# Kernel tuning notes

Measured on AMD Instinct MI355X. Metric: run time of the kernel, lower is better.

The kernel has to match this reference:

```python
import jax, jax.numpy as jnp
import numpy as np

NEG_SLOPE = 0.2


def gat_layer(x, src, dst, W, a_src, a_dst, bias, num_nodes, concat):
    """PyG-style GATConv (eval mode, self-loops already included in src/dst).
    x: [N, F_in]; W: [F_in, H*C]; a_src, a_dst: [H, C]; bias: [H*C] or [C].
    """
    H, C = a_src.shape
    h = (x @ W).reshape(num_nodes, H, C)                    # [N,H,C]
    alpha_s = jnp.einsum('nhc,hc->nh', h, a_src)            # [N,H]
    alpha_d = jnp.einsum('nhc,hc->nh', h, a_dst)            # [N,H]
    e = alpha_s[src] + alpha_d[dst]                         # [E,H]
    e = jnp.where(e > 0, e, NEG_SLOPE * e)                  # LeakyReLU(0.2)
    # segment softmax over destination nodes (numerically stable)
    m = jax.ops.segment_max(e, dst, num_segments=num_nodes)  # [N,H]
    m = jnp.where(jnp.isfinite(m), m, 0.0)
    ex = jnp.exp(e - m[dst])                                # [E,H]
    s = jax.ops.segment_sum(ex, dst, num_segments=num_nodes)  # [N,H]
    alpha = ex / (s[dst] + 1e-16)                           # [E,H]
    msg = h[src] * alpha[:, :, None]                        # [E,H,C]
    out = jax.ops.segment_sum(msg, dst, num_segments=num_nodes)  # [N,H,C]
    if concat:
        out = out.reshape(num_nodes, H * C)
    else:
        out = out.mean(axis=1)
    return out + bias


def _forward(x, edge_index, W1, a_src1, a_dst1, b1, W2, a_src2, a_dst2, b2):
    N = x.shape[0]
    loops = jnp.arange(N, dtype=edge_index.dtype)
    src = jnp.concatenate([edge_index[0], loops])
    dst = jnp.concatenate([edge_index[1], loops])
    h = gat_layer(x, src, dst, W1, a_src1, a_dst1, b1, N, concat=True)
    h = jax.nn.relu(h)  # dropout inactive in eval
    h = gat_layer(h, src, dst, W2, a_src2, a_dst2, b2, N, concat=False)
    return jax.nn.log_softmax(h, axis=1)


def setup_inputs() -> dict:
    key = jax.random.key(0)
    ks = jax.random.split(key, 10)
    N, E, F_in, Hid, H1, F_out = 100000, 1600000, 128, 64, 2, 7
    x = jax.random.normal(ks[0], (N, F_in), dtype=jnp.float32)
    edge_index = jax.random.randint(ks[1], (2, E), 0, N, dtype=jnp.int64)
    s1 = 1.0 / np.sqrt(F_in)
    W1 = jax.random.uniform(ks[2], (F_in, H1 * Hid), jnp.float32, -s1, s1)
    a_src1 = jax.random.uniform(ks[3], (H1, Hid), jnp.float32, -s1, s1)
    a_dst1 = jax.random.uniform(ks[4], (H1, Hid), jnp.float32, -s1, s1)
    b1 = jnp.zeros((H1 * Hid,), jnp.float32)
    s2 = 1.0 / np.sqrt(H1 * Hid)
    W2 = jax.random.uniform(ks[5], (H1 * Hid, F_out), jnp.float32, -s2, s2)
    a_src2 = jax.random.uniform(ks[6], (1, F_out), jnp.float32, -s2, s2)
    a_dst2 = jax.random.uniform(ks[7], (1, F_out), jnp.float32, -s2, s2)
    b2 = jnp.zeros((F_out,), jnp.float32)
    return {"x": x, "edge_index": edge_index, "W1": W1, "a_src1": a_src1,
            "a_dst1": a_dst1, "b1": b1, "W2": W2, "a_src2": a_src2,
            "a_dst2": a_dst2, "b2": b2}


def reference(x, edge_index, W1, a_src1, a_dst1, b1, W2, a_src2, a_dst2, b2):
    return _forward(x, edge_index, W1, a_src1, a_dst1, b1, W2, a_src2, a_dst2, b2)
```

## Files before the change

kernel.cpp:

```cpp
#include <hip/hip_runtime.h>
#include <hip/hip_bf16.h>

#define F_IN 128
#define HC   128
#define C1   64
#define F_OUT 7
#define H2S  8
#define BSH  9
#define BSZ  512
#define BINCH 8192
#define BCAP 12288

typedef __attribute__((ext_vector_type(8))) short short8;
typedef __attribute__((ext_vector_type(4))) float f32x4;
typedef __attribute__((ext_vector_type(2))) float f32x2;

__device__ __forceinline__ ushort f2bf(float f) {
    uint u = __builtin_bit_cast(uint, f);
    u = (u + 0x7FFFu + ((u >> 16) & 1u)) >> 16;
    return (ushort)u;
}

__device__ __forceinline__ int perm_col(int p_byte) {
    int slp = p_byte >> 3, j = p_byte & 7;
    int h = slp >> 3, sg = slp & 7;
    int lr = 2 * sg + (j >> 2), jj = j & 3;
    return 16 * (4 * h + jj) + lr;
}

__global__ __launch_bounds__(256) void k_cvt(
    const float* __restrict__ W1, ushort* __restrict__ Wsw,
    const float* __restrict__ W2, const float* __restrict__ b1,
    float* __restrict__ W2p, float* __restrict__ b1p)
{
    int b = blockIdx.x, t = threadIdx.x;
    if (b < 64) {
        int i = b * 256 + t;
        int k = i >> 7, n = i & 127;
        float v = W1[k * HC + n];
        int idx = n * 128 + (((k & ~7) ^ ((n & 7) << 3)) | (k & 7));
        Wsw[idx] = f2bf(v);
    } else {
        for (int i = t; i < 128 * F_OUT; i += 256) {
            int p = i / F_OUT, o = i - p * F_OUT;
            W2p[i] = W2[perm_col(p) * F_OUT + o];
        }
        if (t < 128) b1p[t] = b1[perm_col(t)];
    }
}

__global__ __launch_bounds__(256) void k_bingemm(
    const int* __restrict__ ei, int E, int Etot, int NBIN,
    int* __restrict__ bcnt, uint* __restrict__ binned,
    const float* __restrict__ x, const ushort* __restrict__ Wsw,
    const float* __restrict__ a_src, const float* __restrict__ a_dst,
    unsigned char* __restrict__ h1p, float* __restrict__ as1, float* __restrict__ ad1,
    int N)
{
    __shared__ __align__(16) char smem[128 * 128 * 2];
    const int t = threadIdx.x;

    if ((int)blockIdx.x < NBIN) {
        int* hist = (int*)smem;
        int* base = hist + 256;
        hist[t] = 0;
        __syncthreads();
        long c0 = (long)blockIdx.x * BINCH;
#pragma unroll
        for (int i = 0; i < BINCH / 256; ++i) {
            long e = c0 + t + i * 256;
            if (e < Etot) {
                int d = (e < E) ? ei[E + e] : (int)(e - E);
                atomicAdd(&hist[d >> BSH], 1);
            }
        }
        __syncthreads();
        base[t] = t * BCAP + ((hist[t] > 0) ? atomicAdd(&bcnt[t], hist[t]) : 0);
        __syncthreads();
#pragma unroll
        for (int i = 0; i < BINCH / 256; ++i) {
            long e = c0 + t + i * 256;
            if (e < Etot) {
                int s, d;
                if (e < E) { s = ei[e]; d = ei[E + e]; } else { s = (int)(e - E); d = s; }
                int bkt = d >> BSH;
                int pos = atomicAdd(&base[bkt], 1);
                if (pos < (bkt + 1) * BCAP)
                    binned[pos] = ((uint)s << BSH) | (uint)(d & (BSZ - 1));
            }
        }
    } else {
        ushort* Bs = (ushort*)smem;
        const int w = t >> 6, l = t & 63;
        const int lr = l & 15, hi = l >> 4;
        const int n0 = (blockIdx.x - NBIN) * 64;

        {
            const uint4* src = (const uint4*)Wsw;
            uint4* dst = (uint4*)Bs;
#pragma unroll
            for (int it = 0; it < 8; ++it) dst[t + it * 256] = src[t + it * 256];
        }
        __syncthreads();

        f32x4 acc[8];
#pragma unroll
        for (int j = 0; j < 8; ++j) acc[j] = (f32x4){0.f, 0.f, 0.f, 0.f};

        int arow = n0 + w * 16 + lr;
        if (arow >= N) arow = N - 1;
        const float* aptr = x + (size_t)arow * F_IN + hi * 8;

#pragma unroll
        for (int kt = 0; kt < 4; ++kt) {
            float4 f0 = *(const float4*)(aptr + kt * 32);
            float4 f1 = *(const float4*)(aptr + kt * 32 + 4);
            short8 a;
            a[0] = (short)f2bf(f0.x); a[1] = (short)f2bf(f0.y);
            a[2] = (short)f2bf(f0.z); a[3] = (short)f2bf(f0.w);
            a[4] = (short)f2bf(f1.x); a[5] = (short)f2bf(f1.y);
            a[6] = (short)f2bf(f1.z); a[7] = (short)f2bf(f1.w);
#pragma unroll
            for (int j = 0; j < 8; ++j) {
                int rn = 16 * j + lr;
                int kidx = (kt * 32 + hi * 8) ^ ((rn & 7) << 3);
                short8 b = *(const short8*)(Bs + rn * 128 + kidx);
                acc[j] = __builtin_amdgcn_mfma_f32_16x16x32_bf16(a, b, acc[j], 0, 0, 0);
            }
        }

        float as_[8], ad_[8];
#pragma unroll
        for (int j = 0; j < 8; ++j) {
            int hd = j >> 2;
            int c = 16 * (j & 3) + lr;
            as_[j] = a_src[hd * C1 + c];
            ad_[j] = a_dst[hd * C1 + c];
        }
#pragma unroll
        for (int i = 0; i < 4; ++i) {
            int r = n0 + w * 16 + hi * 4 + i;
            float ps0 = 0, ps1 = 0, pd0 = 0, pd1 = 0;
#pragma unroll
            for (int j = 0; j < 4; ++j) { ps0 += acc[j][i] * as_[j]; pd0 += acc[j][i] * ad_[j]; }
#pragma unroll
            for (int j = 4; j < 8; ++j) { ps1 += acc[j][i] * as_[j]; pd1 += acc[j][i] * ad_[j]; }
#pragma unroll
            for (int off = 1; off <= 8; off <<= 1) {
                ps0 += __shfl_xor(ps0, off, 64);
                ps1 += __shfl_xor(ps1, off, 64);
                pd0 += __shfl_xor(pd0, off, 64);
                pd1 += __shfl_xor(pd1, off, 64);
            }
            if (r < N) {
                int w0 = 0, w1 = 0;
                w0 = __builtin_amdgcn_cvt_pk_fp8_f32(acc[0][i], acc[1][i], w0, false);
                w0 = __builtin_amdgcn_cvt_pk_fp8_f32(acc[2][i], acc[3][i], w0, true);
                w1 = __builtin_amdgcn_cvt_pk_fp8_f32(acc[4][i], acc[5][i], w1, false);
                w1 = __builtin_amdgcn_cvt_pk_fp8_f32(acc[6][i], acc[7][i], w1, true);
                *(uint*)(h1p + (size_t)r * HC + lr * 4)      = (uint)w0;
                *(uint*)(h1p + (size_t)r * HC + 64 + lr * 4) = (uint)w1;
                if (lr == 0) {
                    as1[r * 2 + 0] = ps0; as1[r * 2 + 1] = ps1;
                    ad1[r * 2 + 0] = pd0; ad1[r * 2 + 1] = pd1;
                }
            }
        }
    }
}

__global__ __launch_bounds__(256) void k_fill(
    const uint* __restrict__ binned, const int* __restrict__ bcnt,
    int* __restrict__ rowptr, int* __restrict__ csr, int N, int NB)
{
    __shared__ int deg[BSZ];
    __shared__ int cur[BSZ];
    __shared__ int sc[256];
    int b = blockIdx.x, t = threadIdx.x;
    int cv = (t < NB) ? min(bcnt[t], BCAP) : 0;
    sc[t] = cv;
    __syncthreads();
    for (int off = 1; off < 256; off <<= 1) {
        int u = (t >= off) ? sc[t - off] : 0;
        __syncthreads();
        sc[t] += u;
        __syncthreads();
    }
    int total = sc[255];
    int s0 = (b > 0) ? sc[b - 1] : 0;
    int cntb = min(bcnt[b], BCAP);
    __syncthreads();

    int n0 = b << BSH;
    int nn = N - n0; if (nn > BSZ) nn = BSZ;
    deg[t] = 0; deg[t + 256] = 0;
    __syncthreads();
    const uint* bb = binned + (size_t)b * BCAP;
    for (int i = t; i < cntb; i += 256)
        atomicAdd(&deg[bb[i] & (BSZ - 1)], 1);
    __syncthreads();
    int d0 = deg[2 * t], d1 = deg[2 * t + 1];
    int ts = d0 + d1;
    sc[t] = ts;
    __syncthreads();
    for (int off = 1; off < 256; off <<= 1) {
        int u = (t >= off) ? sc[t - off] : 0;
        __syncthreads();
        sc[t] += u;
        __syncthreads();
    }
    int ex = sc[t] - ts + s0;
    if (2 * t < nn)     { rowptr[n0 + 2 * t]     = ex;      cur[2 * t]     = ex; }
    if (2 * t + 1 < nn) { rowptr[n0 + 2 * t + 1] = ex + d0; cur[2 * t + 1] = ex + d0; }
    __syncthreads();
    for (int i = t; i < cntb; i += 256) {
        uint en = bb[i];
        int pos = atomicAdd(&cur[en & (BSZ - 1)], 1);
        csr[pos] = (int)(en >> BSH);
    }
    if (b == 0 && t == 0) rowptr[N] = total;
}

__global__ __launch_bounds__(256) void k_aggr1_l2(
    const int* __restrict__ rowptr, const int* __restrict__ csr_src,
    const float* __restrict__ as1, const float* __restrict__ ad1,
    const unsigned char* __restrict__ h1p, const float* __restrict__ b1p,
    const float* __restrict__ W2p, const float* __restrict__ a_src2,
    const float* __restrict__ a_dst2,
    float* __restrict__ h2p, float* __restrict__ as2, float* __restrict__ ad2,
    int N)
{
    int w = threadIdx.x >> 6, l = threadIdx.x & 63;
    int q = l >> 4, sl = l & 15;
    int n = blockIdx.x * 16 + w * 4 + q;
    if (n >= N) return;
    const int h = sl >> 3;
    const int boff = sl * 8;
    float adv = ad1[n * 2 + h];
    int beg = rowptr[n], end = rowptr[n + 1];
    f32x2 ac01 = {0.f, 0.f}, ac23 = {0.f, 0.f}, ac45 = {0.f, 0.f}, ac67 = {0.f, 0.f};
    float s = 0.f;

    int i = beg;
    for (; i + 4 <= end; i += 4) {
        int sv[4]; float Av[4]; uint2 Hv[4];
#pragma unroll
        for (int j = 0; j < 4; ++j) sv[j] = csr_src[i + j];
#pragma unroll
        for (int j = 0; j < 4; ++j) Av[j] = as1[sv[j] * 2 + h];
#pragma unroll
        for (int j = 0; j < 4; ++j)
            Hv[j] = *(const uint2*)(h1p + (((size_t)(uint)sv[j]) << 7) + boff);
#pragma unroll
        for (int j = 0; j < 4; ++j) {
            float a = Av[j] + adv; a = a > 0.f ? a : 0.2f * a;
            float e = __expf(a);
            s += e;
            f32x2 ev = {e, e};
            ac01 += ev * __builtin_amdgcn_cvt_pk_f32_fp8((int)Hv[j].x, false);
            ac23 += ev * __builtin_amdgcn_cvt_pk_f32_fp8((int)Hv[j].x, true);
            ac45 += ev * __builtin_amdgcn_cvt_pk_f32_fp8((int)Hv[j].y, false);
            ac67 += ev * __builtin_amdgcn_cvt_pk_f32_fp8((int)Hv[j].y, true);
        }
    }
    for (; i < end; ++i) {
        int src = csr_src[i];
        float a = as1[src * 2 + h] + adv; a = a > 0.f ? a : 0.2f * a;
        float e = __expf(a);
        s += e;
        uint2 hv = *(const uint2*)(h1p + (((size_t)(uint)src) << 7) + boff);
        f32x2 ev = {e, e};
        ac01 += ev * __builtin_amdgcn_cvt_pk_f32_fp8((int)hv.x, false);
        ac23 += ev * __builtin_amdgcn_cvt_pk_f32_fp8((int)hv.x, true);
        ac45 += ev * __builtin_amdgcn_cvt_pk_f32_fp8((int)hv.y, false);
        ac67 += ev * __builtin_amdgcn_cvt_pk_f32_fp8((int)hv.y, true);
    }
    float inv = 1.f / (s + 1e-16f);

    float4 bv0 = *(const float4*)&b1p[sl * 8];
    float4 bv1 = *(const float4*)&b1p[sl * 8 + 4];
    float v[8];
    v[0] = fmaxf(ac01[0] * inv + bv0.x, 0.f);
    v[1] = fmaxf(ac01[1] * inv + bv0.y, 0.f);
    v[2] = fmaxf(ac23[0] * inv + bv0.z, 0.f);
    v[3] = fmaxf(ac23[1] * inv + bv0.w, 0.f);
    v[4] = fmaxf(ac45[0] * inv + bv1.x, 0.f);
    v[5] = fmaxf(ac45[1] * inv + bv1.y, 0.f);
    v[6] = fmaxf(ac67[0] * inv + bv1.z, 0.f);
    v[7] = fmaxf(ac67[1] * inv + bv1.w, 0.f);

    float w2r[56];
    {
        const float4* wp = (const float4*)(W2p + sl * 56);
#pragma unroll
        for (int k = 0; k < 14; ++k) {
            float4 f = wp[k];
            w2r[4 * k + 0] = f.x; w2r[4 * k + 1] = f.y;
            w2r[4 * k + 2] = f.z; w2r[4 * k + 3] = f.w;
        }
    }
    float p[7];
#pragma unroll
    for (int j = 0; j < 7; ++j) p[j] = 0.f;
#pragma unroll
    for (int r = 0; r < 8; ++r)
#pragma unroll
        for (int j = 0; j < 7; ++j) p[j] += v[r] * w2r[r * 7 + j];
#pragma unroll
    for (int off = 1; off <= 8; off <<= 1)
#pragma unroll
        for (int j = 0; j < 7; ++j) p[j] += __shfl_xor(p[j], off, 64);

    if (sl == 0) {
        float asv = 0.f, adv2 = 0.f;
#pragma unroll
        for (int j = 0; j < 7; ++j) {
            h2p[(size_t)n * H2S + j] = p[j];
            asv += p[j] * a_src2[j];
            adv2 += p[j] * a_dst2[j];
        }
        h2p[(size_t)n * H2S + 7] = 0.f;
        as2[n] = asv; ad2[n] = adv2;
    }
}

__global__ __launch_bounds__(256) void k_aggr2ls(
    const int* __restrict__ rowptr, const int* __restrict__ csr_src,
    const float* __restrict__ as2, const float* __restrict__ ad2,
    const float* __restrict__ h2p, const float* __restrict__ b2,
    float* __restrict__ out, int N)
{
    int g = blockIdx.x * blockDim.x + threadIdx.x;
    int n = g >> 2, l = g & 3;
    if (n >= N) return;
    float adv = ad2[n];
    int beg = rowptr[n], end = rowptr[n + 1];
    f32x2 acc = {0.f, 0.f};
    float s = 0.f;
    int i = beg;
    for (; i + 4 <= end; i += 4) {
        int sv[4]; float Av[4]; float2 Hv[4];
#pragma unroll
        for (int j = 0; j < 4; ++j) sv[j] = csr_src[i + j];
#pragma unroll
        for (int j = 0; j < 4; ++j) Av[j] = as2[sv[j]];
#pragma unroll
        for (int j = 0; j < 4; ++j)
            Hv[j] = *(const float2*)(h2p + ((size_t)(uint)sv[j]) * H2S + 2 * l);
#pragma unroll
        for (int j = 0; j < 4; ++j) {
            float a = Av[j] + adv;
            a = a > 0.f ? a : 0.2f * a;
            float e = __expf(a);
            s += e;
            f32x2 ev = {e, e};
            f32x2 hv = {Hv[j].x, Hv[j].y};
            acc += ev * hv;
        }
    }
    for (; i < end; ++i) {
        int s0 = csr_src[i];
        float a = as2[s0] + adv;
        a = a > 0.f ? a : 0.2f * a;
        float e = __expf(a);
        s += e;
        float2 hv2 = *(const float2*)(h2p + ((size_t)(uint)s0) * H2S + 2 * l);
        f32x2 ev = {e, e};
        f32x2 hv = {hv2.x, hv2.y};
        acc += ev * hv;
    }
    float invs = 1.f / (s + 1e-16f);
    float va = acc[0] * invs + b2[2 * l];
    float vb = (2 * l + 1 < 7) ? acc[1] * invs + b2[2 * l + 1] : -1e30f;
    float m = fmaxf(va, vb);
#pragma unroll
    for (int off = 1; off <= 2; off <<= 1)
        m = fmaxf(m, __shfl_xor(m, off, 4));
    float ex = __expf(va - m) + ((2 * l + 1 < 7) ? __expf(vb - m) : 0.f);
#pragma unroll
    for (int off = 1; off <= 2; off <<= 1)
        ex += __shfl_xor(ex, off, 4);
    float lg = __logf(ex);
    out[(size_t)n * F_OUT + 2 * l] = va - m - lg;
    if (2 * l + 1 < 7) out[(size_t)n * F_OUT + 2 * l + 1] = vb - m - lg;
}

extern "C" void kernel_launch(void* const* d_in, const int* in_sizes, int n_in,
                              void* d_out, int out_size, void* d_ws, size_t ws_size,
                              hipStream_t stream) {
    const float* x      = (const float*)d_in[0];
    const int*   ei     = (const int*)d_in[1];
    const float* W1     = (const float*)d_in[2];
    const float* a_src1 = (const float*)d_in[3];
    const float* a_dst1 = (const float*)d_in[4];
    const float* b1     = (const float*)d_in[5];
    const float* W2     = (const float*)d_in[6];
    const float* a_src2 = (const float*)d_in[7];
    const float* a_dst2 = (const float*)d_in[8];
    const float* b2     = (const float*)d_in[9];
    float* out = (float*)d_out;

    const int N    = in_sizes[0] / F_IN;
    const int E    = in_sizes[1] / 2;
    const int Etot = E + N;
    const int NB   = (N + BSZ - 1) >> BSH;
    const int NBIN = (Etot + BINCH - 1) / BINCH;

    char* ws = (char*)d_ws;
    size_t off = 0;
    auto A = [&](size_t bytes) -> void* {
        char* p = ws + off;
        off += (bytes + 255) & ~(size_t)255;
        return (void*)p;
    };
    ushort* Wsw    = (ushort*)A((size_t)128 * 128 * 2);
    float*  W2p    = (float*) A((size_t)128 * F_OUT * 4);
    float*  b1p    = (float*) A((size_t)128 * 4);
    unsigned char* h1p = (unsigned char*)A((size_t)N * HC);
    float*  as1    = (float*) A((size_t)N * 2 * 4);
    float*  ad1    = (float*) A((size_t)N * 2 * 4);
    int*    rowptr = (int*)   A((size_t)(N + 1) * 4);
    int*    csr    = (int*)   A((size_t)Etot * 4);
    int*    bcnt   = (int*)   A(256 * 4);
    uint*   binned = (uint*)  A((size_t)NB * BCAP * 4);
    float*  h2p    = (float*)binned;
    float*  as2    = (float*)((char*)binned + (((size_t)N * H2S * 4 + 255) & ~(size_t)255));
    float*  ad2    = (float*)((char*)as2 + (((size_t)N * 4 + 255) & ~(size_t)255));

    hipMemsetAsync(bcnt, 0, 256 * 4, stream);

    k_cvt<<<65, 256, 0, stream>>>(W1, Wsw, W2, b1, W2p, b1p);
    k_bingemm<<<NBIN + (N + 63) / 64, 256, 0, stream>>>(
        ei, E, Etot, NBIN, bcnt, binned,
        x, Wsw, a_src1, a_dst1, h1p, as1, ad1, N);
    k_fill<<<NB, 256, 0, stream>>>(binned, bcnt, rowptr, csr, N, NB);
    k_aggr1_l2<<<(N + 15) / 16, 256, 0, stream>>>(rowptr, csr, as1, ad1, h1p,
                                                  b1p, W2p, a_src2, a_dst2,
                                                  h2p, as2, ad2, N);
    k_aggr2ls<<<((size_t)N * 4 + 255) / 256, 256, 0, stream>>>(rowptr, csr,
                                                               as2, ad2, h2p, b2, out, N);
}
```

Measured before the change: 148.9 us.

## Cache edge reads in registers, pack as2 into h2 padding, drop memset

The binning pass now reads each edge once, keeps the packed value and bucket in registers between the histogram and scatter phases, and halves the chunk size so more blocks run. The layer-2 source attention score is stored in the unused eighth slot of h2 and fetched with a lane shuffle, which removes a separate random gather per edge. The bcnt memset is folded into k_cvt to save one launch. Risks: more registers per thread in the binning blocks, and NBIN must match the new chunk size on the host side.

```diff
diff --git a/kernel.cpp b/kernel.cpp
--- a/kernel.cpp
+++ b/kernel.cpp
@@ -8,7 +8,7 @@
 #define H2S  8
 #define BSH  9
 #define BSZ  512
-#define BINCH 8192
+#define BINCH 4096
 #define BCAP 12288
 
 typedef __attribute__((ext_vector_type(8))) short short8;
@@ -31,7 +31,7 @@
 __global__ __launch_bounds__(256) void k_cvt(
     const float* __restrict__ W1, ushort* __restrict__ Wsw,
     const float* __restrict__ W2, const float* __restrict__ b1,
-    float* __restrict__ W2p, float* __restrict__ b1p)
+    float* __restrict__ W2p, float* __restrict__ b1p, int* __restrict__ bcnt)
 {
     int b = blockIdx.x, t = threadIdx.x;
     if (b < 64) {
@@ -41,6 +41,7 @@
         int idx = n * 128 + (((k & ~7) ^ ((n & 7) << 3)) | (k & 7));
         Wsw[idx] = f2bf(v);
     } else {
+        bcnt[t] = 0;
         for (int i = t; i < 128 * F_OUT; i += 256) {
             int p = i / F_OUT, o = i - p * F_OUT;
             W2p[i] = W2[perm_col(p) * F_OUT + o];
@@ -66,27 +67,28 @@
         hist[t] = 0;
         __syncthreads();
         long c0 = (long)blockIdx.x * BINCH;
-#pragma unroll
-        for (int i = 0; i < BINCH / 256; ++i) {
-            long e = c0 + t + i * 256;
+        uint val[16]; int bkt[16];
+#pragma unroll
+        for (int i2 = 0; i2 < 16; ++i2) {
+            long e = c0 + t + i2 * 256;
+            int s = 0, d = 0;
+            bkt[i2] = -1;
             if (e < Etot) {
-                int d = (e < E) ? ei[E + e] : (int)(e - E);
-                atomicAdd(&hist[d >> BSH], 1);
+                if (e < E) { s = ei[e]; d = ei[E + e]; } else { s = (int)(e - E); d = s; }
+                bkt[i2] = d >> BSH;
+                atomicAdd(&hist[bkt[i2]], 1);
             }
+            val[i2] = ((uint)s << BSH) | (uint)(d & (BSZ - 1));
         }
         __syncthreads();
         base[t] = t * BCAP + ((hist[t] > 0) ? atomicAdd(&bcnt[t], hist[t]) : 0);
         __syncthreads();
 #pragma unroll
-        for (int i = 0; i < BINCH / 256; ++i) {
-            long e = c0 + t + i * 256;
-            if (e < Etot) {
-                int s, d;
-                if (e < E) { s = ei[e]; d = ei[E + e]; } else { s = (int)(e - E); d = s; }
-                int bkt = d >> BSH;
-                int pos = atomicAdd(&base[bkt], 1);
-                if (pos < (bkt + 1) * BCAP)
-                    binned[pos] = ((uint)s << BSH) | (uint)(d & (BSZ - 1));
+        for (int i2 = 0; i2 < 16; ++i2) {
+            if (bkt[i2] >= 0) {
+                int pos = atomicAdd(&base[bkt[i2]], 1);
+                if (pos < (bkt[i2] + 1) * BCAP)
+                    binned[pos] = val[i2];
             }
         }
     } else {
@@ -227,7 +229,7 @@
     const unsigned char* __restrict__ h1p, const float* __restrict__ b1p,
     const float* __restrict__ W2p, const float* __restrict__ a_src2,
     const float* __restrict__ a_dst2,
-    float* __restrict__ h2p, float* __restrict__ as2, float* __restrict__ ad2,
+    float* __restrict__ h2p, float* __restrict__ ad2,
     int N)
 {
     int w = threadIdx.x >> 6, l = threadIdx.x & 63;
@@ -319,19 +321,20 @@
             asv += p[j] * a_src2[j];
             adv2 += p[j] * a_dst2[j];
         }
-        h2p[(size_t)n * H2S + 7] = 0.f;
-        as2[n] = asv; ad2[n] = adv2;
+        h2p[(size_t)n * H2S + 7] = asv;
+        ad2[n] = adv2;
     }
 }
 
 __global__ __launch_bounds__(256) void k_aggr2ls(
     const int* __restrict__ rowptr, const int* __restrict__ csr_src,
-    const float* __restrict__ as2, const float* __restrict__ ad2,
+    const float* __restrict__ ad2,
     const float* __restrict__ h2p, const float* __restrict__ b2,
     float* __restrict__ out, int N)
 {
     int g = blockIdx.x * blockDim.x + threadIdx.x;
-    int n = g >> 2, l = g & 3;
+    int n = g >> 2, l = g & 2 | (g & 1);
+    l = g & 3;
     if (n >= N) return;
     float adv = ad2[n];
     int beg = rowptr[n], end = rowptr[n + 1];
@@ -339,17 +342,16 @@
     float s = 0.f;
     int i = beg;
     for (; i + 4 <= end; i += 4) {
-        int sv[4]; float Av[4]; float2 Hv[4];
+        int sv[4]; float2 Hv[4];
 #pragma unroll
         for (int j = 0; j < 4; ++j) sv[j] = csr_src[i + j];
-#pragma unroll
-        for (int j = 0; j < 4; ++j) Av[j] = as2[sv[j]];
 #pragma unroll
         for (int j = 0; j < 4; ++j)
             Hv[j] = *(const float2*)(h2p + ((size_t)(uint)sv[j]) * H2S + 2 * l);
 #pragma unroll
         for (int j = 0; j < 4; ++j) {
-            float a = Av[j] + adv;
+            float as2v = __shfl(Hv[j].y, 3, 4);
+            float a = as2v + adv;
             a = a > 0.f ? a : 0.2f * a;
             float e = __expf(a);
             s += e;
@@ -360,11 +362,12 @@
     }
     for (; i < end; ++i) {
         int s0 = csr_src[i];
-        float a = as2[s0] + adv;
+        float2 hv2 = *(const float2*)(h2p + ((size_t)(uint)s0) * H2S + 2 * l);
+        float as2v = __shfl(hv2.y, 3, 4);
+        float a = as2v + adv;
         a = a > 0.f ? a : 0.2f * a;
         float e = __expf(a);
         s += e;
-        float2 hv2 = *(const float2*)(h2p + ((size_t)(uint)s0) * H2S + 2 * l);
         f32x2 ev = {e, e};
         f32x2 hv = {hv2.x, hv2.y};
         acc += ev * hv;
@@ -424,19 +427,16 @@
     int*    bcnt   = (int*)   A(256 * 4);
     uint*   binned = (uint*)  A((size_t)NB * BCAP * 4);
     float*  h2p    = (float*)binned;
-    float*  as2    = (float*)((char*)binned + (((size_t)N * H2S * 4 + 255) & ~(size_t)255));
-    float*  ad2    = (float*)((char*)as2 + (((size_t)N * 4 + 255) & ~(size_t)255));
-
-    hipMemsetAsync(bcnt, 0, 256 * 4, stream);
-
-    k_cvt<<<65, 256, 0, stream>>>(W1, Wsw, W2, b1, W2p, b1p);
+    float*  ad2    = (float*)((char*)binned + (((size_t)N * H2S * 4 + 255) & ~(size_t)255));
+
+    k_cvt<<<65, 256, 0, stream>>>(W1, Wsw, W2, b1, W2p, b1p, bcnt);
     k_bingemm<<<NBIN + (N + 63) / 64, 256, 0, stream>>>(
         ei, E, Etot, NBIN, bcnt, binned,
         x, Wsw, a_src1, a_dst1, h1p, as1, ad1, N);
     k_fill<<<NB, 256, 0, stream>>>(binned, bcnt, rowptr, csr, N, NB);
     k_aggr1_l2<<<(N + 15) / 16, 256, 0, stream>>>(rowptr, csr, as1, ad1, h1p,
                                                   b1p, W2p, a_src2, a_dst2,
-                                                  h2p, as2, ad2, N);
+                                                  h2p, ad2, N);
     k_aggr2ls<<<((size_t)N * 4 + 255) / 256, 256, 0, stream>>>(rowptr, csr,
-                                                               as2, ad2, h2p, b2, out, N);
-}
+                                                               ad2, h2p, b2, out, N);
+}
```

After: 134.6 us. -9.6%, faster.
